# Performance work log

Measured on AMD Instinct MI355X. Metric: run time of the kernel, lower is better.

The kernel has to match this reference:

```python
import jax, jax.numpy as jnp
import numpy as np


def setup_inputs() -> dict:
    key = jax.random.key(0)
    kq, kk, kv = jax.random.split(key, 3)
    B, L, S, H, E = 2, 2048, 2048, 16, 64
    queries = jax.random.normal(kq, (B, L, H, E), dtype=jnp.float32)
    keys = jax.random.normal(kk, (B, S, H, E), dtype=jnp.float32)
    values = jax.random.normal(kv, (B, S, H, E), dtype=jnp.float32)
    # TriangularCausalMask: True strictly above the diagonal (positions to mask)
    causal = jnp.triu(jnp.ones((L, S), dtype=jnp.bool_), k=1)
    attn_mask = jnp.broadcast_to(causal[None, None, :, :], (B, 1, L, S))
    return {"queries": queries, "keys": keys, "values": values, "attn_mask": attn_mask}


def reference(queries, keys, values, attn_mask):
    # queries: [B,L,H,E], keys/values: [B,S,H,E], attn_mask: [B,1,L,S] bool
    E = queries.shape[-1]
    scale = 1.0 / jnp.sqrt(jnp.asarray(E, dtype=queries.dtype))
    scores = jnp.einsum('blhe,bshe->bhls', queries, keys)      # [B,H,L,S]
    scores = jnp.where(attn_mask, -jnp.inf, scores)
    A = jax.nn.softmax(scale * scores, axis=-1)                # dropout is identity in eval
    V = jnp.einsum('bhls,bshd->blhd', A, values)               # [B,L,H,D]
    return V, A
```

## Files before the change

### kernel.cpp

```cpp
#include <hip/hip_runtime.h>
#include <hip/hip_bf16.h>


#define B_ 2
#define L_ 2048
#define S_ 2048
#define H_ 16
#define E_ 64
#define HE 1024
#define KP 72
#define PP 68

typedef __attribute__((ext_vector_type(8))) __bf16 bfrag;
typedef __attribute__((ext_vector_type(4))) float f32x4;

__device__ __forceinline__ unsigned short f2bu(float x) {
    __bf16 b = (__bf16)x;
    return __builtin_bit_cast(unsigned short, b);
}

__global__ __launch_bounds__(256, 4)
void fullattn_kernel(const float* __restrict__ Qg,
                     const float* __restrict__ Kg,
                     const float* __restrict__ Vg,
                     float* __restrict__ Vout,
                     float* __restrict__ Aout)
{
    __shared__ __align__(16) __bf16 Ks[64 * KP];
    __shared__ __align__(16) __bf16 Vt[64 * KP];
    __shared__ __align__(16) float  Pw[4][16 * PP];

    const int tid  = threadIdx.x;
    const int wave = tid >> 6;
    const int lane = tid & 63;
    const int ln   = lane & 15;
    const int quad = lane >> 4;
    const int lq   = quad * 4;

    const int bx = blockIdx.x;
    const int qt = (bx & 1) ? (31 - (bx >> 1)) : (bx >> 1);
    const int bh = blockIdx.y;
    const int b  = bh >> 4;
    const int h  = bh & 15;

    const int q0  = qt * 64;
    const int q0w = q0 + wave * 16;

    const float* qbase = Qg + ((size_t)b * L_ * H_ + h) * E_;
    const float* kbase = Kg + ((size_t)b * S_ * H_ + h) * E_;
    const float* vbase = Vg + ((size_t)b * S_ * H_ + h) * E_;
    float* arow0 = Aout + (size_t)bh * L_ * S_;

    bfrag qf[2];
    {
        const float* qr = qbase + (size_t)(q0w + ln) * HE;
        #pragma unroll
        for (int kc = 0; kc < 2; ++kc) {
            const float* p = qr + kc * 32 + quad * 8;
            float4 a0 = *(const float4*)(p);
            float4 a1 = *(const float4*)(p + 4);
            bfrag f;
            f[0] = (__bf16)(a0.x * 0.125f); f[1] = (__bf16)(a0.y * 0.125f);
            f[2] = (__bf16)(a0.z * 0.125f); f[3] = (__bf16)(a0.w * 0.125f);
            f[4] = (__bf16)(a1.x * 0.125f); f[5] = (__bf16)(a1.y * 0.125f);
            f[6] = (__bf16)(a1.z * 0.125f); f[7] = (__bf16)(a1.w * 0.125f);
            qf[kc] = f;
        }
    }

    const int r  = tid >> 2;
    const int c0 = tid & 3;

    float lsum[4] = {0.f, 0.f, 0.f, 0.f};

    float4 kpre[4];
    {
        const float* kr = kbase + (size_t)r * HE;
        #pragma unroll
        for (int i = 0; i < 4; ++i)
            kpre[i] = *(const float4*)(kr + (c0 + i * 4) * 4);
    }

    for (int st = 0; st <= qt; ++st) {
        __syncthreads();
        #pragma unroll
        for (int i = 0; i < 4; ++i) {
            int f4 = c0 + i * 4;
            ushort4 kb;
            kb.x = f2bu(kpre[i].x); kb.y = f2bu(kpre[i].y);
            kb.z = f2bu(kpre[i].z); kb.w = f2bu(kpre[i].w);
            *(ushort4*)&Ks[r * KP + f4 * 4] = kb;
        }
        if (st < qt) {
            const float* kr = kbase + (size_t)((st + 1) * 64 + r) * HE;
            #pragma unroll
            for (int i = 0; i < 4; ++i)
                kpre[i] = *(const float4*)(kr + (c0 + i * 4) * 4);
        }
        __syncthreads();
        #pragma unroll
        for (int nc = 0; nc < 4; ++nc) {
            f32x4 acc = {0.f, 0.f, 0.f, 0.f};
            __builtin_amdgcn_s_setprio(1);
            #pragma unroll
            for (int kc = 0; kc < 2; ++kc) {
                bfrag bk = *(const bfrag*)&Ks[(nc * 16 + ln) * KP + kc * 32 + quad * 8];
                acc = __builtin_amdgcn_mfma_f32_16x16x32_bf16(qf[kc], bk, acc, 0, 0, 0);
            }
            __builtin_amdgcn_s_setprio(0);
            const int s_abs = st * 64 + nc * 16 + ln;
            #pragma unroll
            for (int rg = 0; rg < 4; ++rg) {
                const int q_abs = q0w + lq + rg;
                float e = (s_abs <= q_abs) ? __expf(acc[rg]) : 0.0f;
                lsum[rg] += e;
            }
        }
    }

    float4 kp2[4], vp2[4];
    {
        const float* kr = kbase + (size_t)r * HE;
        const float* vr = vbase + (size_t)r * HE;
        #pragma unroll
        for (int i = 0; i < 4; ++i) {
            kp2[i] = *(const float4*)(kr + (c0 + i * 4) * 4);
            vp2[i] = *(const float4*)(vr + (c0 + i * 4) * 4);
        }
    }

    float inv_l[4];
    #pragma unroll
    for (int rg = 0; rg < 4; ++rg) {
        float v = lsum[rg];
        v += __shfl_xor(v, 1);
        v += __shfl_xor(v, 2);
        v += __shfl_xor(v, 4);
        v += __shfl_xor(v, 8);
        inv_l[rg] = 1.0f / v;
    }

    f32x4 oacc[4];
    #pragma unroll
    for (int dc = 0; dc < 4; ++dc) {
        f32x4 z = {0.f, 0.f, 0.f, 0.f};
        oacc[dc] = z;
    }

    const int wr = lane >> 2;
    const int wc = (lane & 3) * 4;

    for (int st = 0; st <= qt; ++st) {
        __syncthreads();
        #pragma unroll
        for (int i = 0; i < 4; ++i) {
            int f4 = c0 + i * 4;
            ushort4 kb;
            kb.x = f2bu(kp2[i].x); kb.y = f2bu(kp2[i].y);
            kb.z = f2bu(kp2[i].z); kb.w = f2bu(kp2[i].w);
            *(ushort4*)&Ks[r * KP + f4 * 4] = kb;
            const int d0 = f4 * 4;
            Vt[(d0 + 0) * KP + r] = (__bf16)vp2[i].x;
            Vt[(d0 + 1) * KP + r] = (__bf16)vp2[i].y;
            Vt[(d0 + 2) * KP + r] = (__bf16)vp2[i].z;
            Vt[(d0 + 3) * KP + r] = (__bf16)vp2[i].w;
        }
        if (st < qt) {
            const float* kr = kbase + (size_t)((st + 1) * 64 + r) * HE;
            const float* vr = vbase + (size_t)((st + 1) * 64 + r) * HE;
            #pragma unroll
            for (int i = 0; i < 4; ++i) {
                kp2[i] = *(const float4*)(kr + (c0 + i * 4) * 4);
                vp2[i] = *(const float4*)(vr + (c0 + i * 4) * 4);
            }
        }
        __syncthreads();

        #pragma unroll
        for (int nc = 0; nc < 4; ++nc) {
            f32x4 acc = {0.f, 0.f, 0.f, 0.f};
            __builtin_amdgcn_s_setprio(1);
            #pragma unroll
            for (int kc = 0; kc < 2; ++kc) {
                bfrag bk = *(const bfrag*)&Ks[(nc * 16 + ln) * KP + kc * 32 + quad * 8];
                acc = __builtin_amdgcn_mfma_f32_16x16x32_bf16(qf[kc], bk, acc, 0, 0, 0);
            }
            __builtin_amdgcn_s_setprio(0);
            const int s_abs = st * 64 + nc * 16 + ln;
            #pragma unroll
            for (int rg = 0; rg < 4; ++rg) {
                const int q_abs = q0w + lq + rg;
                float e = (s_abs <= q_abs) ? __expf(acc[rg]) : 0.0f;
                Pw[wave][(lq + rg) * PP + nc * 16 + ln] = e * inv_l[rg];
            }
        }

        bfrag af[2];
        #pragma unroll
        for (int kc = 0; kc < 2; ++kc) {
            const float* pp = &Pw[wave][ln * PP + kc * 32 + quad * 8];
            float4 p0 = *(const float4*)pp;
            float4 p1 = *(const float4*)(pp + 4);
            bfrag f;
            f[0] = (__bf16)p0.x; f[1] = (__bf16)p0.y;
            f[2] = (__bf16)p0.z; f[3] = (__bf16)p0.w;
            f[4] = (__bf16)p1.x; f[5] = (__bf16)p1.y;
            f[6] = (__bf16)p1.z; f[7] = (__bf16)p1.w;
            af[kc] = f;
        }

        #pragma unroll
        for (int dc = 0; dc < 4; ++dc) {
            __builtin_amdgcn_s_setprio(1);
            #pragma unroll
            for (int kc = 0; kc < 2; ++kc) {
                bfrag bv = *(const bfrag*)&Vt[(dc * 16 + ln) * KP + kc * 32 + quad * 8];
                oacc[dc] = __builtin_amdgcn_mfma_f32_16x16x32_bf16(af[kc], bv, oacc[dc], 0, 0, 0);
            }
            __builtin_amdgcn_s_setprio(0);
        }

        float* ar = arow0 + (size_t)(q0w + wr) * S_ + st * 64;
        #pragma unroll
        for (int c4 = 0; c4 < 4; ++c4) {
            float4 v4 = *(const float4*)&Pw[wave][wr * PP + wc + c4 * 16];
            *(float4*)(ar + wc + c4 * 16) = v4;
        }
    }

    {
        const float4 z4 = {0.f, 0.f, 0.f, 0.f};
        for (int st = qt + 1; st < S_ / 64; ++st) {
            float* ar = arow0 + (size_t)(q0w + wr) * S_ + st * 64;
            #pragma unroll
            for (int c4 = 0; c4 < 4; ++c4)
                *(float4*)(ar + wc + c4 * 16) = z4;
        }
    }

    #pragma unroll
    for (int rg = 0; rg < 4; ++rg) {
        float* vr = Vout + ((size_t)(b * L_ + q0w + lq + rg) * H_ + h) * E_;
        #pragma unroll
        for (int dc = 0; dc < 4; ++dc)
            vr[dc * 16 + ln] = oacc[dc][rg];
    }
}

extern "C" void kernel_launch(void* const* d_in, const int* in_sizes, int n_in,
                              void* d_out, int out_size, void* d_ws, size_t ws_size,
                              hipStream_t stream) {
    const float* Q = (const float*)d_in[0];
    const float* K = (const float*)d_in[1];
    const float* V = (const float*)d_in[2];
    float* out  = (float*)d_out;
    float* Vo   = out;
    float* Ao   = out + (size_t)B_ * L_ * H_ * E_;
    dim3 grid(L_ / 64, B_ * H_);
    fullattn_kernel<<<grid, 256, 0, stream>>>(Q, K, V, Vo, Ao);
}
```

Baseline: 725.8 us.

## Pair complementary causal query tiles in one 512-thread block sharing K/V tiles

```diff
diff --git a/kernel.cpp b/kernel.cpp
--- a/kernel.cpp
+++ b/kernel.cpp
@@ -10,6 +10,7 @@
 #define HE 1024
 #define KP 72
 #define PP 68
+#define NT 32
 
 typedef __attribute__((ext_vector_type(8))) __bf16 bfrag;
 typedef __attribute__((ext_vector_type(4))) float f32x4;
@@ -19,7 +20,13 @@
     return __builtin_bit_cast(unsigned short, b);
 }
 
-__global__ __launch_bounds__(256, 4)
+__device__ __forceinline__ void barrier_nodrain() {
+    asm volatile("s_waitcnt lgkmcnt(0)" ::: "memory");
+    __builtin_amdgcn_s_barrier();
+    __builtin_amdgcn_sched_barrier(0);
+}
+
+__global__ __launch_bounds__(512, 4)
 void fullattn_kernel(const float* __restrict__ Qg,
                      const float* __restrict__ Kg,
                      const float* __restrict__ Vg,
@@ -28,23 +35,25 @@
 {
     __shared__ __align__(16) __bf16 Ks[64 * KP];
     __shared__ __align__(16) __bf16 Vt[64 * KP];
-    __shared__ __align__(16) float  Pw[4][16 * PP];
+    __shared__ __align__(16) float  Pw[8][16 * PP];
 
     const int tid  = threadIdx.x;
     const int wave = tid >> 6;
+    const int half = wave >> 2;
+    const int wv   = wave & 3;
     const int lane = tid & 63;
     const int ln   = lane & 15;
     const int quad = lane >> 4;
     const int lq   = quad * 4;
 
-    const int bx = blockIdx.x;
-    const int qt = (bx & 1) ? (31 - (bx >> 1)) : (bx >> 1);
-    const int bh = blockIdx.y;
-    const int b  = bh >> 4;
-    const int h  = bh & 15;
-
-    const int q0  = qt * 64;
-    const int q0w = q0 + wave * 16;
+    const int p   = blockIdx.x;
+    const int qt  = half ? (NT - 1 - p) : p;
+    const int qtB = NT - 1 - p;
+    const int bh  = blockIdx.y;
+    const int b   = bh >> 4;
+    const int h   = bh & 15;
+
+    const int q0w = qt * 64 + wv * 16;
 
     const float* qbase = Qg + ((size_t)b * L_ * H_ + h) * E_;
     const float* kbase = Kg + ((size_t)b * S_ * H_ + h) * E_;
@@ -56,9 +65,9 @@
         const float* qr = qbase + (size_t)(q0w + ln) * HE;
         #pragma unroll
         for (int kc = 0; kc < 2; ++kc) {
-            const float* p = qr + kc * 32 + quad * 8;
-            float4 a0 = *(const float4*)(p);
-            float4 a1 = *(const float4*)(p + 4);
+            const float* pq = qr + kc * 32 + quad * 8;
+            float4 a0 = *(const float4*)(pq);
+            float4 a1 = *(const float4*)(pq + 4);
             bfrag f;
             f[0] = (__bf16)(a0.x * 0.125f); f[1] = (__bf16)(a0.y * 0.125f);
             f[2] = (__bf16)(a0.z * 0.125f); f[3] = (__bf16)(a0.w * 0.125f);
@@ -68,64 +77,67 @@
         }
     }
 
-    const int r  = tid >> 2;
-    const int c0 = tid & 3;
+    const int r  = tid >> 3;
+    const int c0 = tid & 7;
 
     float lsum[4] = {0.f, 0.f, 0.f, 0.f};
 
-    float4 kpre[4];
+    float4 kpre[2];
     {
         const float* kr = kbase + (size_t)r * HE;
         #pragma unroll
-        for (int i = 0; i < 4; ++i)
-            kpre[i] = *(const float4*)(kr + (c0 + i * 4) * 4);
-    }
-
-    for (int st = 0; st <= qt; ++st) {
-        __syncthreads();
-        #pragma unroll
-        for (int i = 0; i < 4; ++i) {
-            int f4 = c0 + i * 4;
+        for (int i = 0; i < 2; ++i)
+            kpre[i] = *(const float4*)(kr + (c0 + i * 8) * 4);
+    }
+
+    for (int st = 0; st <= qtB; ++st) {
+        #pragma unroll
+        for (int i = 0; i < 2; ++i) {
+            int f4 = c0 + i * 8;
             ushort4 kb;
             kb.x = f2bu(kpre[i].x); kb.y = f2bu(kpre[i].y);
             kb.z = f2bu(kpre[i].z); kb.w = f2bu(kpre[i].w);
             *(ushort4*)&Ks[r * KP + f4 * 4] = kb;
         }
-        if (st < qt) {
+        if (st < qtB) {
             const float* kr = kbase + (size_t)((st + 1) * 64 + r) * HE;
             #pragma unroll
-            for (int i = 0; i < 4; ++i)
-                kpre[i] = *(const float4*)(kr + (c0 + i * 4) * 4);
-        }
-        __syncthreads();
-        #pragma unroll
-        for (int nc = 0; nc < 4; ++nc) {
-            f32x4 acc = {0.f, 0.f, 0.f, 0.f};
-            __builtin_amdgcn_s_setprio(1);
-            #pragma unroll
-            for (int kc = 0; kc < 2; ++kc) {
-                bfrag bk = *(const bfrag*)&Ks[(nc * 16 + ln) * KP + kc * 32 + quad * 8];
-                acc = __builtin_amdgcn_mfma_f32_16x16x32_bf16(qf[kc], bk, acc, 0, 0, 0);
-            }
-            __builtin_amdgcn_s_setprio(0);
-            const int s_abs = st * 64 + nc * 16 + ln;
-            #pragma unroll
-            for (int rg = 0; rg < 4; ++rg) {
-                const int q_abs = q0w + lq + rg;
-                float e = (s_abs <= q_abs) ? __expf(acc[rg]) : 0.0f;
-                lsum[rg] += e;
-            }
-        }
-    }
-
-    float4 kp2[4], vp2[4];
+            for (int i = 0; i < 2; ++i)
+                kpre[i] = *(const float4*)(kr + (c0 + i * 8) * 4);
+        }
+        barrier_nodrain();
+
+        if (st <= qt) {
+            #pragma unroll
+            for (int nc = 0; nc < 4; ++nc) {
+                f32x4 acc = {0.f, 0.f, 0.f, 0.f};
+                __builtin_amdgcn_s_setprio(1);
+                #pragma unroll
+                for (int kc = 0; kc < 2; ++kc) {
+                    bfrag bk = *(const bfrag*)&Ks[(nc * 16 + ln) * KP + kc * 32 + quad * 8];
+                    acc = __builtin_amdgcn_mfma_f32_16x16x32_bf16(qf[kc], bk, acc, 0, 0, 0);
+                }
+                __builtin_amdgcn_s_setprio(0);
+                const int s_abs = st * 64 + nc * 16 + ln;
+                #pragma unroll
+                for (int rg = 0; rg < 4; ++rg) {
+                    const int q_abs = q0w + lq + rg;
+                    float e = (s_abs <= q_abs) ? __expf(acc[rg]) : 0.0f;
+                    lsum[rg] += e;
+                }
+            }
+        }
+        barrier_nodrain();
+    }
+
+    float4 kp2[2], vp2[2];
     {
         const float* kr = kbase + (size_t)r * HE;
         const float* vr = vbase + (size_t)r * HE;
         #pragma unroll
-        for (int i = 0; i < 4; ++i) {
-            kp2[i] = *(const float4*)(kr + (c0 + i * 4) * 4);
-            vp2[i] = *(const float4*)(vr + (c0 + i * 4) * 4);
+        for (int i = 0; i < 2; ++i) {
+            kp2[i] = *(const float4*)(kr + (c0 + i * 8) * 4);
+            vp2[i] = *(const float4*)(vr + (c0 + i * 8) * 4);
         }
     }
 
@@ -149,12 +161,12 @@
 
     const int wr = lane >> 2;
     const int wc = (lane & 3) * 4;
-
-    for (int st = 0; st <= qt; ++st) {
-        __syncthreads();
-        #pragma unroll
-        for (int i = 0; i < 4; ++i) {
-            int f4 = c0 + i * 4;
+    int zf = qt + 1;
+
+    for (int st = 0; st <= qtB; ++st) {
+        #pragma unroll
+        for (int i = 0; i < 2; ++i) {
+            int f4 = c0 + i * 8;
             ushort4 kb;
             kb.x = f2bu(kp2[i].x); kb.y = f2bu(kp2[i].y);
             kb.z = f2bu(kp2[i].z); kb.w = f2bu(kp2[i].w);
@@ -165,73 +177,82 @@
             Vt[(d0 + 2) * KP + r] = (__bf16)vp2[i].z;
             Vt[(d0 + 3) * KP + r] = (__bf16)vp2[i].w;
         }
-        if (st < qt) {
+        if (st < qtB) {
             const float* kr = kbase + (size_t)((st + 1) * 64 + r) * HE;
             const float* vr = vbase + (size_t)((st + 1) * 64 + r) * HE;
             #pragma unroll
-            for (int i = 0; i < 4; ++i) {
-                kp2[i] = *(const float4*)(kr + (c0 + i * 4) * 4);
-                vp2[i] = *(const float4*)(vr + (c0 + i * 4) * 4);
-            }
-        }
-        __syncthreads();
-
-        #pragma unroll
-        for (int nc = 0; nc < 4; ++nc) {
-            f32x4 acc = {0.f, 0.f, 0.f, 0.f};
-            __builtin_amdgcn_s_setprio(1);
+            for (int i = 0; i < 2; ++i) {
+                kp2[i] = *(const float4*)(kr + (c0 + i * 8) * 4);
+                vp2[i] = *(const float4*)(vr + (c0 + i * 8) * 4);
+            }
+        }
+        barrier_nodrain();
+
+        if (st <= qt) {
+            #pragma unroll
+            for (int nc = 0; nc < 4; ++nc) {
+                f32x4 acc = {0.f, 0.f, 0.f, 0.f};
+                __builtin_amdgcn_s_setprio(1);
+                #pragma unroll
+                for (int kc = 0; kc < 2; ++kc) {
+                    bfrag bk = *(const bfrag*)&Ks[(nc * 16 + ln) * KP + kc * 32 + quad * 8];
+                    acc = __builtin_amdgcn_mfma_f32_16x16x32_bf16(qf[kc], bk, acc, 0, 0, 0);
+                }
+                __builtin_amdgcn_s_setprio(0);
+                const int s_abs = st * 64 + nc * 16 + ln;
+                #pragma unroll
+                for (int rg = 0; rg < 4; ++rg) {
+                    const int q_abs = q0w + lq + rg;
+                    float e = (s_abs <= q_abs) ? __expf(acc[rg]) : 0.0f;
+                    Pw[wave][(lq + rg) * PP + nc * 16 + ln] = e * inv_l[rg];
+                }
+            }
+            bfrag af[2];
             #pragma unroll
             for (int kc = 0; kc < 2; ++kc) {
-                bfrag bk = *(const bfrag*)&Ks[(nc * 16 + ln) * KP + kc * 32 + quad * 8];
-                acc = __builtin_amdgcn_mfma_f32_16x16x32_bf16(qf[kc], bk, acc, 0, 0, 0);
-            }
-            __builtin_amdgcn_s_setprio(0);
-            const int s_abs = st * 64 + nc * 16 + ln;
-            #pragma unroll
-            for (int rg = 0; rg < 4; ++rg) {
-                const int q_abs = q0w + lq + rg;
-                float e = (s_abs <= q_abs) ? __expf(acc[rg]) : 0.0f;
-                Pw[wave][(lq + rg) * PP + nc * 16 + ln] = e * inv_l[rg];
-            }
-        }
-
-        bfrag af[2];
-        #pragma unroll
-        for (int kc = 0; kc < 2; ++kc) {
-            const float* pp = &Pw[wave][ln * PP + kc * 32 + quad * 8];
-            float4 p0 = *(const float4*)pp;
-            float4 p1 = *(const float4*)(pp + 4);
-            bfrag f;
-            f[0] = (__bf16)p0.x; f[1] = (__bf16)p0.y;
-            f[2] = (__bf16)p0.z; f[3] = (__bf16)p0.w;
-            f[4] = (__bf16)p1.x; f[5] = (__bf16)p1.y;
-            f[6] = (__bf16)p1.z; f[7] = (__bf16)p1.w;
-            af[kc] = f;
-        }
-
-        #pragma unroll
-        for (int dc = 0; dc < 4; ++dc) {
-            __builtin_amdgcn_s_setprio(1);
-            #pragma unroll
-            for (int kc = 0; kc < 2; ++kc) {
-                bfrag bv = *(const bfrag*)&Vt[(dc * 16 + ln) * KP + kc * 32 + quad * 8];
-                oacc[dc] = __builtin_amdgcn_mfma_f32_16x16x32_bf16(af[kc], bv, oacc[dc], 0, 0, 0);
-            }
-            __builtin_amdgcn_s_setprio(0);
-        }
-
-        float* ar = arow0 + (size_t)(q0w + wr) * S_ + st * 64;
-        #pragma unroll
-        for (int c4 = 0; c4 < 4; ++c4) {
-            float4 v4 = *(const float4*)&Pw[wave][wr * PP + wc + c4 * 16];
-            *(float4*)(ar + wc + c4 * 16) = v4;
-        }
+                const float* pp = &Pw[wave][ln * PP + kc * 32 + quad * 8];
+                float4 p0 = *(const float4*)pp;
+                float4 p1 = *(const float4*)(pp + 4);
+                bfrag f;
+                f[0] = (__bf16)p0.x; f[1] = (__bf16)p0.y;
+                f[2] = (__bf16)p0.z; f[3] = (__bf16)p0.w;
+                f[4] = (__bf16)p1.x; f[5] = (__bf16)p1.y;
+                f[6] = (__bf16)p1.z; f[7] = (__bf16)p1.w;
+                af[kc] = f;
+            }
+
+            #pragma unroll
+            for (int dc = 0; dc < 4; ++dc) {
+                __builtin_amdgcn_s_setprio(1);
+                #pragma unroll
+                for (int kc = 0; kc < 2; ++kc) {
+                    bfrag bv = *(const bfrag*)&Vt[(dc * 16 + ln) * KP + kc * 32 + quad * 8];
+                    oacc[dc] = __builtin_amdgcn_mfma_f32_16x16x32_bf16(af[kc], bv, oacc[dc], 0, 0, 0);
+                }
+                __builtin_amdgcn_s_setprio(0);
+            }
+
+            float* ar = arow0 + (size_t)(q0w + wr) * S_ + st * 64;
+            #pragma unroll
+            for (int c4 = 0; c4 < 4; ++c4) {
+                float4 v4 = *(const float4*)&Pw[wave][wr * PP + wc + c4 * 16];
+                *(float4*)(ar + wc + c4 * 16) = v4;
+            }
+        } else if (zf < NT) {
+            const float4 z4 = {0.f, 0.f, 0.f, 0.f};
+            float* ar = arow0 + (size_t)(q0w + wr) * S_ + zf * 64;
+            #pragma unroll
+            for (int c4 = 0; c4 < 4; ++c4)
+                *(float4*)(ar + wc + c4 * 16) = z4;
+            ++zf;
+        }
+        barrier_nodrain();
     }
 
     {
         const float4 z4 = {0.f, 0.f, 0.f, 0.f};
-        for (int st = qt + 1; st < S_ / 64; ++st) {
-            float* ar = arow0 + (size_t)(q0w + wr) * S_ + st * 64;
+        for (; zf < NT; ++zf) {
+            float* ar = arow0 + (size_t)(q0w + wr) * S_ + zf * 64;
             #pragma unroll
             for (int c4 = 0; c4 < 4; ++c4)
                 *(float4*)(ar + wc + c4 * 16) = z4;
@@ -256,6 +277,6 @@
     float* out  = (float*)d_out;
     float* Vo   = out;
     float* Ao   = out + (size_t)B_ * L_ * H_ * E_;
-    dim3 grid(L_ / 64, B_ * H_);
-    fullattn_kernel<<<grid, 256, 0, stream>>>(Q, K, V, Vo, Ao);
-}
+    dim3 grid(NT / 2, B_ * H_);
+    fullattn_kernel<<<grid, 512, 0, stream>>>(Q, K, V, Vo, Ao);
+}
```

New measurement: 667.3 us. -8.1%, faster.

## Pair causal query tiles per block and split KV tiles across two wave groups

Applied to the files above, without the earlier changes.

```diff
diff --git a/kernel.cpp b/kernel.cpp
--- a/kernel.cpp
+++ b/kernel.cpp
@@ -10,6 +10,7 @@
 #define HE 1024
 #define KP 72
 #define PP 68
+#define NT 32
 
 typedef __attribute__((ext_vector_type(8))) __bf16 bfrag;
 typedef __attribute__((ext_vector_type(4))) float f32x4;
@@ -19,231 +20,298 @@
     return __builtin_bit_cast(unsigned short, b);
 }
 
-__global__ __launch_bounds__(256, 4)
+__device__ __forceinline__ void barrier_nodrain() {
+    asm volatile("s_waitcnt lgkmcnt(0)" ::: "memory");
+    __builtin_amdgcn_s_barrier();
+    __builtin_amdgcn_sched_barrier(0);
+}
+
+__global__ __launch_bounds__(512, 4)
 void fullattn_kernel(const float* __restrict__ Qg,
                      const float* __restrict__ Kg,
                      const float* __restrict__ Vg,
                      float* __restrict__ Vout,
                      float* __restrict__ Aout)
 {
-    __shared__ __align__(16) __bf16 Ks[64 * KP];
-    __shared__ __align__(16) __bf16 Vt[64 * KP];
-    __shared__ __align__(16) float  Pw[4][16 * PP];
+    __shared__ __align__(16) __bf16 Ks[2][64 * KP];
+    __shared__ __align__(16) __bf16 Vt[2][64 * KP];
+    __shared__ __align__(16) float  Pw[8][16 * PP];
+    __shared__ float Lred[8][16];
 
     const int tid  = threadIdx.x;
     const int wave = tid >> 6;
+    const int sub  = wave >> 2;
+    const int wq   = wave & 3;
     const int lane = tid & 63;
     const int ln   = lane & 15;
     const int quad = lane >> 4;
     const int lq   = quad * 4;
 
-    const int bx = blockIdx.x;
-    const int qt = (bx & 1) ? (31 - (bx >> 1)) : (bx >> 1);
+    const int p  = blockIdx.x;
     const int bh = blockIdx.y;
     const int b  = bh >> 4;
     const int h  = bh & 15;
-
-    const int q0  = qt * 64;
-    const int q0w = q0 + wave * 16;
 
     const float* qbase = Qg + ((size_t)b * L_ * H_ + h) * E_;
     const float* kbase = Kg + ((size_t)b * S_ * H_ + h) * E_;
     const float* vbase = Vg + ((size_t)b * S_ * H_ + h) * E_;
     float* arow0 = Aout + (size_t)bh * L_ * S_;
 
-    bfrag qf[2];
-    {
-        const float* qr = qbase + (size_t)(q0w + ln) * HE;
-        #pragma unroll
-        for (int kc = 0; kc < 2; ++kc) {
-            const float* p = qr + kc * 32 + quad * 8;
-            float4 a0 = *(const float4*)(p);
-            float4 a1 = *(const float4*)(p + 4);
-            bfrag f;
-            f[0] = (__bf16)(a0.x * 0.125f); f[1] = (__bf16)(a0.y * 0.125f);
-            f[2] = (__bf16)(a0.z * 0.125f); f[3] = (__bf16)(a0.w * 0.125f);
-            f[4] = (__bf16)(a1.x * 0.125f); f[5] = (__bf16)(a1.y * 0.125f);
-            f[6] = (__bf16)(a1.z * 0.125f); f[7] = (__bf16)(a1.w * 0.125f);
-            qf[kc] = f;
-        }
-    }
-
-    const int r  = tid >> 2;
-    const int c0 = tid & 3;
-
-    float lsum[4] = {0.f, 0.f, 0.f, 0.f};
-
-    float4 kpre[4];
-    {
-        const float* kr = kbase + (size_t)r * HE;
-        #pragma unroll
-        for (int i = 0; i < 4; ++i)
-            kpre[i] = *(const float4*)(kr + (c0 + i * 4) * 4);
-    }
-
-    for (int st = 0; st <= qt; ++st) {
-        __syncthreads();
-        #pragma unroll
-        for (int i = 0; i < 4; ++i) {
-            int f4 = c0 + i * 4;
-            ushort4 kb;
-            kb.x = f2bu(kpre[i].x); kb.y = f2bu(kpre[i].y);
-            kb.z = f2bu(kpre[i].z); kb.w = f2bu(kpre[i].w);
-            *(ushort4*)&Ks[r * KP + f4 * 4] = kb;
-        }
-        if (st < qt) {
-            const float* kr = kbase + (size_t)((st + 1) * 64 + r) * HE;
+    const int hf = tid >> 8;
+    const int ht = tid & 255;
+    const int r  = ht >> 2;
+    const int c0 = ht & 3;
+
+    const int wr = lane >> 2;
+    const int wc = (lane & 3) * 4;
+
+    int zi = wave;
+
+    #pragma unroll 1
+    for (int pass = 0; pass < 2; ++pass) {
+        const int qt  = pass ? p : (NT - 1 - p);
+        const int nt  = qt + 1;
+        const int nph = (nt + 1) >> 1;
+        const int q0w = qt * 64 + wq * 16;
+
+        bfrag qf[2];
+        {
+            const float* qr = qbase + (size_t)(q0w + ln) * HE;
+            #pragma unroll
+            for (int kc = 0; kc < 2; ++kc) {
+                const float* pq = qr + kc * 32 + quad * 8;
+                float4 a0 = *(const float4*)(pq);
+                float4 a1 = *(const float4*)(pq + 4);
+                bfrag f;
+                f[0] = (__bf16)(a0.x * 0.125f); f[1] = (__bf16)(a0.y * 0.125f);
+                f[2] = (__bf16)(a0.z * 0.125f); f[3] = (__bf16)(a0.w * 0.125f);
+                f[4] = (__bf16)(a1.x * 0.125f); f[5] = (__bf16)(a1.y * 0.125f);
+                f[6] = (__bf16)(a1.z * 0.125f); f[7] = (__bf16)(a1.w * 0.125f);
+                qf[kc] = f;
+            }
+        }
+
+        float lsum[4] = {0.f, 0.f, 0.f, 0.f};
+        float4 kpre[4];
+        {
+            const float* kr = kbase + (size_t)(hf * 64 + r) * HE;
             #pragma unroll
             for (int i = 0; i < 4; ++i)
                 kpre[i] = *(const float4*)(kr + (c0 + i * 4) * 4);
         }
-        __syncthreads();
+
+        for (int ph = 0; ph < nph; ++ph) {
+            #pragma unroll
+            for (int i = 0; i < 4; ++i) {
+                int f4 = c0 + i * 4;
+                ushort4 kb;
+                kb.x = f2bu(kpre[i].x); kb.y = f2bu(kpre[i].y);
+                kb.z = f2bu(kpre[i].z); kb.w = f2bu(kpre[i].w);
+                *(ushort4*)&Ks[hf][r * KP + f4 * 4] = kb;
+            }
+            if (ph + 1 < nph) {
+                const float* kr = kbase + (size_t)((2 * (ph + 1) + hf) * 64 + r) * HE;
+                #pragma unroll
+                for (int i = 0; i < 4; ++i)
+                    kpre[i] = *(const float4*)(kr + (c0 + i * 4) * 4);
+            }
+            barrier_nodrain();
+
+            const int tmy = 2 * ph + sub;
+            if (tmy < nt) {
+                #pragma unroll
+                for (int nc = 0; nc < 4; ++nc) {
+                    f32x4 acc = {0.f, 0.f, 0.f, 0.f};
+                    __builtin_amdgcn_s_setprio(1);
+                    #pragma unroll
+                    for (int kc = 0; kc < 2; ++kc) {
+                        bfrag bk = *(const bfrag*)&Ks[sub][(nc * 16 + ln) * KP + kc * 32 + quad * 8];
+                        acc = __builtin_amdgcn_mfma_f32_16x16x32_bf16(qf[kc], bk, acc, 0, 0, 0);
+                    }
+                    __builtin_amdgcn_s_setprio(0);
+                    const int s_abs = tmy * 64 + nc * 16 + ln;
+                    #pragma unroll
+                    for (int rg = 0; rg < 4; ++rg) {
+                        const int q_abs = q0w + lq + rg;
+                        float e = (s_abs <= q_abs) ? __expf(acc[rg]) : 0.0f;
+                        lsum[rg] += e;
+                    }
+                }
+            }
+            if (pass == 0 && zi < NT - 1) {
+                const int i = zi; zi += 8;
+                int r0, tile;
+                if (i < p) { r0 = (NT - 1 - p) * 64; tile = NT - p + i; }
+                else       { r0 = p * 64;            tile = p + 1 + (i - p); }
+                const float4 z4 = {0.f, 0.f, 0.f, 0.f};
+                float* ab = arow0 + (size_t)(r0 + wr) * S_ + tile * 64 + wc;
+                #pragma unroll
+                for (int rr = 0; rr < 4; ++rr) {
+                    float* ar = ab + (size_t)(rr * 16) * S_;
+                    #pragma unroll
+                    for (int c4 = 0; c4 < 4; ++c4)
+                        *(float4*)(ar + c4 * 16) = z4;
+                }
+            }
+            barrier_nodrain();
+        }
+
+        float vred[4];
         #pragma unroll
-        for (int nc = 0; nc < 4; ++nc) {
-            f32x4 acc = {0.f, 0.f, 0.f, 0.f};
-            __builtin_amdgcn_s_setprio(1);
-            #pragma unroll
-            for (int kc = 0; kc < 2; ++kc) {
-                bfrag bk = *(const bfrag*)&Ks[(nc * 16 + ln) * KP + kc * 32 + quad * 8];
-                acc = __builtin_amdgcn_mfma_f32_16x16x32_bf16(qf[kc], bk, acc, 0, 0, 0);
-            }
-            __builtin_amdgcn_s_setprio(0);
-            const int s_abs = st * 64 + nc * 16 + ln;
-            #pragma unroll
-            for (int rg = 0; rg < 4; ++rg) {
-                const int q_abs = q0w + lq + rg;
-                float e = (s_abs <= q_abs) ? __expf(acc[rg]) : 0.0f;
-                lsum[rg] += e;
-            }
-        }
-    }
-
-    float4 kp2[4], vp2[4];
-    {
-        const float* kr = kbase + (size_t)r * HE;
-        const float* vr = vbase + (size_t)r * HE;
+        for (int rg = 0; rg < 4; ++rg) {
+            float v = lsum[rg];
+            v += __shfl_xor(v, 1);
+            v += __shfl_xor(v, 2);
+            v += __shfl_xor(v, 4);
+            v += __shfl_xor(v, 8);
+            vred[rg] = v;
+        }
+        if (ln == 0) {
+            #pragma unroll
+            for (int rg = 0; rg < 4; ++rg)
+                Lred[wave][lq + rg] = vred[rg];
+        }
+        barrier_nodrain();
+        float inv_l[4];
         #pragma unroll
-        for (int i = 0; i < 4; ++i) {
-            kp2[i] = *(const float4*)(kr + (c0 + i * 4) * 4);
-            vp2[i] = *(const float4*)(vr + (c0 + i * 4) * 4);
-        }
-    }
-
-    float inv_l[4];
-    #pragma unroll
-    for (int rg = 0; rg < 4; ++rg) {
-        float v = lsum[rg];
-        v += __shfl_xor(v, 1);
-        v += __shfl_xor(v, 2);
-        v += __shfl_xor(v, 4);
-        v += __shfl_xor(v, 8);
-        inv_l[rg] = 1.0f / v;
-    }
-
-    f32x4 oacc[4];
-    #pragma unroll
-    for (int dc = 0; dc < 4; ++dc) {
-        f32x4 z = {0.f, 0.f, 0.f, 0.f};
-        oacc[dc] = z;
-    }
-
-    const int wr = lane >> 2;
-    const int wc = (lane & 3) * 4;
-
-    for (int st = 0; st <= qt; ++st) {
-        __syncthreads();
+        for (int rg = 0; rg < 4; ++rg)
+            inv_l[rg] = 1.0f / (Lred[wq][lq + rg] + Lred[wq + 4][lq + rg]);
+
+        f32x4 oacc[4];
         #pragma unroll
-        for (int i = 0; i < 4; ++i) {
-            int f4 = c0 + i * 4;
-            ushort4 kb;
-            kb.x = f2bu(kp2[i].x); kb.y = f2bu(kp2[i].y);
-            kb.z = f2bu(kp2[i].z); kb.w = f2bu(kp2[i].w);
-            *(ushort4*)&Ks[r * KP + f4 * 4] = kb;
-            const int d0 = f4 * 4;
-            Vt[(d0 + 0) * KP + r] = (__bf16)vp2[i].x;
-            Vt[(d0 + 1) * KP + r] = (__bf16)vp2[i].y;
-            Vt[(d0 + 2) * KP + r] = (__bf16)vp2[i].z;
-            Vt[(d0 + 3) * KP + r] = (__bf16)vp2[i].w;
-        }
-        if (st < qt) {
-            const float* kr = kbase + (size_t)((st + 1) * 64 + r) * HE;
-            const float* vr = vbase + (size_t)((st + 1) * 64 + r) * HE;
+        for (int dc = 0; dc < 4; ++dc) {
+            f32x4 z = {0.f, 0.f, 0.f, 0.f};
+            oacc[dc] = z;
+        }
+
+        float4 kp2[4], vp2[4];
+        {
+            const float* kr = kbase + (size_t)(hf * 64 + r) * HE;
+            const float* vr = vbase + (size_t)(hf * 64 + r) * HE;
             #pragma unroll
             for (int i = 0; i < 4; ++i) {
                 kp2[i] = *(const float4*)(kr + (c0 + i * 4) * 4);
                 vp2[i] = *(const float4*)(vr + (c0 + i * 4) * 4);
             }
         }
-        __syncthreads();
-
+
+        for (int ph = 0; ph < nph; ++ph) {
+            #pragma unroll
+            for (int i = 0; i < 4; ++i) {
+                int f4 = c0 + i * 4;
+                ushort4 kb;
+                kb.x = f2bu(kp2[i].x); kb.y = f2bu(kp2[i].y);
+                kb.z = f2bu(kp2[i].z); kb.w = f2bu(kp2[i].w);
+                *(ushort4*)&Ks[hf][r * KP + f4 * 4] = kb;
+                const int d0 = f4 * 4;
+                Vt[hf][(d0 + 0) * KP + r] = (__bf16)vp2[i].x;
+                Vt[hf][(d0 + 1) * KP + r] = (__bf16)vp2[i].y;
+                Vt[hf][(d0 + 2) * KP + r] = (__bf16)vp2[i].z;
+                Vt[hf][(d0 + 3) * KP + r] = (__bf16)vp2[i].w;
+            }
+            if (ph + 1 < nph) {
+                const float* kr = kbase + (size_t)((2 * (ph + 1) + hf) * 64 + r) * HE;
+                const float* vr = vbase + (size_t)((2 * (ph + 1) + hf) * 64 + r) * HE;
+                #pragma unroll
+                for (int i = 0; i < 4; ++i) {
+                    kp2[i] = *(const float4*)(kr + (c0 + i * 4) * 4);
+                    vp2[i] = *(const float4*)(vr + (c0 + i * 4) * 4);
+                }
+            }
+            barrier_nodrain();
+
+            const int tmy = 2 * ph + sub;
+            if (tmy < nt) {
+                #pragma unroll
+                for (int nc = 0; nc < 4; ++nc) {
+                    f32x4 acc = {0.f, 0.f, 0.f, 0.f};
+                    __builtin_amdgcn_s_setprio(1);
+                    #pragma unroll
+                    for (int kc = 0; kc < 2; ++kc) {
+                        bfrag bk = *(const bfrag*)&Ks[sub][(nc * 16 + ln) * KP + kc * 32 + quad * 8];
+                        acc = __builtin_amdgcn_mfma_f32_16x16x32_bf16(qf[kc], bk, acc, 0, 0, 0);
+                    }
+                    __builtin_amdgcn_s_setprio(0);
+                    const int s_abs = tmy * 64 + nc * 16 + ln;
+                    #pragma unroll
+                    for (int rg = 0; rg < 4; ++rg) {
+                        const int q_abs = q0w + lq + rg;
+                        float e = (s_abs <= q_abs) ? __expf(acc[rg]) : 0.0f;
+                        Pw[wave][(lq + rg) * PP + nc * 16 + ln] = e * inv_l[rg];
+                    }
+                }
+                bfrag af[2];
+                #pragma unroll
+                for (int kc = 0; kc < 2; ++kc) {
+                    const float* pp = &Pw[wave][ln * PP + kc * 32 + quad * 8];
+                    float4 p0 = *(const float4*)pp;
+                    float4 p1 = *(const float4*)(pp + 4);
+                    bfrag f;
+                    f[0] = (__bf16)p0.x; f[1] = (__bf16)p0.y;
+                    f[2] = (__bf16)p0.z; f[3] = (__bf16)p0.w;
+                    f[4] = (__bf16)p1.x; f[5] = (__bf16)p1.y;
+                    f[6] = (__bf16)p1.z; f[7] = (__bf16)p1.w;
+                    af[kc] = f;
+                }
+                #pragma unroll
+                for (int dc = 0; dc < 4; ++dc) {
+                    __builtin_amdgcn_s_setprio(1);
+                    #pragma unroll
+                    for (int kc = 0; kc < 2; ++kc) {
+                        bfrag bv = *(const bfrag*)&Vt[sub][(dc * 16 + ln) * KP + kc * 32 + quad * 8];
+                        oacc[dc] = __builtin_amdgcn_mfma_f32_16x16x32_bf16(af[kc], bv, oacc[dc], 0, 0, 0);
+                    }
+                    __builtin_amdgcn_s_setprio(0);
+                }
+                float* ar = arow0 + (size_t)(q0w + wr) * S_ + tmy * 64;
+                #pragma unroll
+                for (int c4 = 0; c4 < 4; ++c4) {
+                    float4 v4 = *(const float4*)&Pw[wave][wr * PP + wc + c4 * 16];
+                    *(float4*)(ar + wc + c4 * 16) = v4;
+                }
+            }
+            barrier_nodrain();
+        }
+
+        if (sub == 1) {
+            #pragma unroll
+            for (int dc = 0; dc < 4; ++dc)
+                #pragma unroll
+                for (int rg = 0; rg < 4; ++rg)
+                    Pw[wave][(lq + rg) * PP + dc * 16 + ln] = oacc[dc][rg];
+        }
+        barrier_nodrain();
+        if (sub == 0) {
+            #pragma unroll
+            for (int dc = 0; dc < 4; ++dc)
+                #pragma unroll
+                for (int rg = 0; rg < 4; ++rg)
+                    oacc[dc][rg] += Pw[wq + 4][(lq + rg) * PP + dc * 16 + ln];
+            #pragma unroll
+            for (int rg = 0; rg < 4; ++rg) {
+                float* vr = Vout + ((size_t)(b * L_ + q0w + lq + rg) * H_ + h) * E_;
+                #pragma unroll
+                for (int dc = 0; dc < 4; ++dc)
+                    vr[dc * 16 + ln] = oacc[dc][rg];
+            }
+        }
+        barrier_nodrain();
+    }
+
+    for (; zi < NT - 1; zi += 8) {
+        const int i = zi;
+        int r0, tile;
+        if (i < p) { r0 = (NT - 1 - p) * 64; tile = NT - p + i; }
+        else       { r0 = p * 64;            tile = p + 1 + (i - p); }
+        const float4 z4 = {0.f, 0.f, 0.f, 0.f};
+        float* ab = arow0 + (size_t)(r0 + wr) * S_ + tile * 64 + wc;
         #pragma unroll
-        for (int nc = 0; nc < 4; ++nc) {
-            f32x4 acc = {0.f, 0.f, 0.f, 0.f};
-            __builtin_amdgcn_s_setprio(1);
-            #pragma unroll
-            for (int kc = 0; kc < 2; ++kc) {
-                bfrag bk = *(const bfrag*)&Ks[(nc * 16 + ln) * KP + kc * 32 + quad * 8];
-                acc = __builtin_amdgcn_mfma_f32_16x16x32_bf16(qf[kc], bk, acc, 0, 0, 0);
-            }
-            __builtin_amdgcn_s_setprio(0);
-            const int s_abs = st * 64 + nc * 16 + ln;
-            #pragma unroll
-            for (int rg = 0; rg < 4; ++rg) {
-                const int q_abs = q0w + lq + rg;
-                float e = (s_abs <= q_abs) ? __expf(acc[rg]) : 0.0f;
-                Pw[wave][(lq + rg) * PP + nc * 16 + ln] = e * inv_l[rg];
-            }
-        }
-
-        bfrag af[2];
-        #pragma unroll
-        for (int kc = 0; kc < 2; ++kc) {
-            const float* pp = &Pw[wave][ln * PP + kc * 32 + quad * 8];
-            float4 p0 = *(const float4*)pp;
-            float4 p1 = *(const float4*)(pp + 4);
-            bfrag f;
-            f[0] = (__bf16)p0.x; f[1] = (__bf16)p0.y;
-            f[2] = (__bf16)p0.z; f[3] = (__bf16)p0.w;
-            f[4] = (__bf16)p1.x; f[5] = (__bf16)p1.y;
-            f[6] = (__bf16)p1.z; f[7] = (__bf16)p1.w;
-            af[kc] = f;
-        }
-
-        #pragma unroll
-        for (int dc = 0; dc < 4; ++dc) {
-            __builtin_amdgcn_s_setprio(1);
-            #pragma unroll
-            for (int kc = 0; kc < 2; ++kc) {
-                bfrag bv = *(const bfrag*)&Vt[(dc * 16 + ln) * KP + kc * 32 + quad * 8];
-                oacc[dc] = __builtin_amdgcn_mfma_f32_16x16x32_bf16(af[kc], bv, oacc[dc], 0, 0, 0);
-            }
-            __builtin_amdgcn_s_setprio(0);
-        }
-
-        float* ar = arow0 + (size_t)(q0w + wr) * S_ + st * 64;
-        #pragma unroll
-        for (int c4 = 0; c4 < 4; ++c4) {
-            float4 v4 = *(const float4*)&Pw[wave][wr * PP + wc + c4 * 16];
-            *(float4*)(ar + wc + c4 * 16) = v4;
-        }
-    }
-
-    {
-        const float4 z4 = {0.f, 0.f, 0.f, 0.f};
-        for (int st = qt + 1; st < S_ / 64; ++st) {
-            float* ar = arow0 + (size_t)(q0w + wr) * S_ + st * 64;
+        for (int rr = 0; rr < 4; ++rr) {
+            float* ar = ab + (size_t)(rr * 16) * S_;
             #pragma unroll
             for (int c4 = 0; c4 < 4; ++c4)
-                *(float4*)(ar + wc + c4 * 16) = z4;
-        }
-    }
-
-    #pragma unroll
-    for (int rg = 0; rg < 4; ++rg) {
-        float* vr = Vout + ((size_t)(b * L_ + q0w + lq + rg) * H_ + h) * E_;
-        #pragma unroll
-        for (int dc = 0; dc < 4; ++dc)
-            vr[dc * 16 + ln] = oacc[dc][rg];
+                *(float4*)(ar + c4 * 16) = z4;
+        }
     }
 }
 
@@ -256,6 +324,6 @@
     float* out  = (float*)d_out;
     float* Vo   = out;
     float* Ao   = out + (size_t)B_ * L_ * H_ * E_;
-    dim3 grid(L_ / 64, B_ * H_);
-    fullattn_kernel<<<grid, 256, 0, stream>>>(Q, K, V, Vo, Ao);
+    dim3 grid(NT / 2, B_ * H_);
+    fullattn_kernel<<<grid, 512, 0, stream>>>(Q, K, V, Vo, Ao);
 }
```

After: 705.7 us. 2.8% less time.
